# Kernel tuning notes

Measured on AMD Instinct MI355X. Metric: run time of the kernel, lower is better.

Reference implementation:

```python
import jax, jax.numpy as jnp
import numpy as np

KS = 3          # deform kernel size
N = KS * KS     # sampling points per output pixel
PAD = 1         # zero padding

def conv2d(x, w, stride, padding):
    return jax.lax.conv_general_dilated(
        x, w, (stride, stride), [(padding, padding), (padding, padding)],
        dimension_numbers=('NCHW', 'OIHW', 'NCHW'))

def _gather(x_flat, qx, qy, Wp):
    # x_flat: [b, c, Hp*Wp]; qx, qy: [b, h, w, N] int32 -> [b, c, h, w, N]
    b = qx.shape[0]; c = x_flat.shape[1]
    idx = (qx * Wp + qy).reshape(b, 1, -1)
    out = jnp.take_along_axis(x_flat, jnp.broadcast_to(idx, (b, c, idx.shape[-1])), axis=2)
    return out.reshape(b, c, qx.shape[1], qx.shape[2], qx.shape[3])

def deform_conv(x, w_off, b_off, w_conv):
    # learned per-pixel offsets: [b, 2N, h, w] (first N = x-offsets, last N = y-offsets)
    offset = conv2d(x, w_off, 1, PAD) + b_off[None, :, None, None]
    b, _, h, w = offset.shape
    x_pad = jnp.pad(x, ((0, 0), (0, 0), (PAD, PAD), (PAD, PAD)))
    Hp, Wp = x_pad.shape[2], x_pad.shape[3]
    # kernel-relative offsets p_n in {-1,0,1}^2
    pn_x, pn_y = jnp.meshgrid(jnp.arange(-(KS // 2), KS // 2 + 1),
                              jnp.arange(-(KS // 2), KS // 2 + 1), indexing='ij')
    p_n = jnp.concatenate([pn_x.reshape(-1), pn_y.reshape(-1)]).reshape(1, 2 * N, 1, 1)
    # base grid p_0 (1..h, 1..w in padded coordinates)
    p0_x, p0_y = jnp.meshgrid(jnp.arange(1, h + 1), jnp.arange(1, w + 1), indexing='ij')
    p_0 = jnp.concatenate([jnp.tile(p0_x[None], (N, 1, 1)),
                           jnp.tile(p0_y[None], (N, 1, 1))])[None]  # [1, 2N, h, w]
    p = (p_0 + p_n).astype(offset.dtype) + offset                   # [b, 2N, h, w]
    p = jnp.transpose(p, (0, 2, 3, 1))                              # [b, h, w, 2N]
    px, py = p[..., :N], p[..., N:]
    q = jnp.floor(jax.lax.stop_gradient(p))
    qlt_x = jnp.clip(q[..., :N], 0, Hp - 1); qlt_y = jnp.clip(q[..., N:], 0, Wp - 1)
    qrb_x = jnp.clip(q[..., :N] + 1, 0, Hp - 1); qrb_y = jnp.clip(q[..., N:] + 1, 0, Wp - 1)
    px = jnp.clip(px, 0, Hp - 1); py = jnp.clip(py, 0, Wp - 1)
    # bilinear weights (classic DCN formulation)
    g_lt = (1 + (qlt_x - px)) * (1 + (qlt_y - py))
    g_rb = (1 - (qrb_x - px)) * (1 - (qrb_y - py))
    g_lb = (1 + (qlt_x - px)) * (1 - (qrb_y - py))
    g_rt = (1 - (qrb_x - px)) * (1 + (qlt_y - py))
    x_flat = x_pad.reshape(b, x_pad.shape[1], -1)
    qi = lambda a: a.astype(jnp.int32)
    x_lt = _gather(x_flat, qi(qlt_x), qi(qlt_y), Wp)
    x_rb = _gather(x_flat, qi(qrb_x), qi(qrb_y), Wp)
    x_lb = _gather(x_flat, qi(qlt_x), qi(qrb_y), Wp)
    x_rt = _gather(x_flat, qi(qrb_x), qi(qlt_y), Wp)
    xo = (g_lt[:, None] * x_lt + g_rb[:, None] * x_rb
          + g_lb[:, None] * x_lb + g_rt[:, None] * x_rt)  # [b, c, h, w, N]
    c = xo.shape[1]
    # unfold N -> (ks, ks) blocks: [b, c, h*ks, w*ks]
    xo = xo.reshape(b, c, h, w, KS, KS).transpose(0, 1, 2, 4, 3, 5).reshape(b, c, h * KS, w * KS)
    return conv2d(xo, w_conv, KS, 0)  # stride=ks aggregation, no bias

def reference(x, w_off, b_off, w_conv, w_fc, b_fc):
    y = jax.nn.relu(deform_conv(x, w_off, b_off, w_conv))          # [b, 8, 28, 28]
    y = jax.lax.reduce_window(y, -jnp.inf, jax.lax.max,
                              (1, 1, 2, 2), (1, 1, 2, 2), 'VALID')  # [b, 8, 14, 14]
    y = y.reshape(y.shape[0], -1)
    return y @ w_fc.T + b_fc

def setup_inputs() -> dict:
    key = jax.random.key(0)
    k1, k2, k3, k4 = jax.random.split(key, 4)
    B = 4096
    return {
        'x': jax.random.normal(k1, (B, 1, 28, 28), dtype=jnp.float32),
        'w_off': jax.random.normal(k2, (18, 1, 3, 3), dtype=jnp.float32) * 0.1,
        'b_off': jnp.zeros((18,), dtype=jnp.float32),
        'w_conv': jax.random.normal(k3, (8, 1, 3, 3), dtype=jnp.float32) * 0.3,
        'w_fc': jax.random.normal(k4, (10, 8 * 14 * 14), dtype=jnp.float32) * 0.02,
        'b_fc': jnp.zeros((10,), dtype=jnp.float32),
    }
```

## Files before the change

### kernel.cpp

```cpp
#include <hip/hip_runtime.h>


#define HH 28
#define WW 28
#define WP 30
#define NPOS 784
#define NPOOL 1568
#define CELLS 196

__global__ __launch_bounds__(256) void deform_net_kernel(
    const float* __restrict__ x,
    const float* __restrict__ w_off,
    const float* __restrict__ b_off,
    const float* __restrict__ w_conv,
    const float* __restrict__ w_fc,
    const float* __restrict__ b_fc,
    float* __restrict__ out)
{
    __shared__ float xs[900];
    __shared__ float wo_s[162];
    __shared__ float bo_s[18];
    __shared__ float wc_s[72];
    __shared__ float red[4][10];

    const int b   = blockIdx.x;
    const int tid = threadIdx.x;

    if (tid < 162) wo_s[tid] = w_off[tid];
    if (tid < 18)  bo_s[tid] = b_off[tid];
    if (tid < 72)  wc_s[tid] = w_conv[tid];

    const float* xb = x + (size_t)b * NPOS;
    for (int i = tid; i < 900; i += 256) {
        int r = i / WP, c = i % WP;
        float v = 0.f;
        if (r >= 1 && r <= HH && c >= 1 && c <= WW)
            v = xb[(r - 1) * WW + (c - 1)];
        xs[i] = v;
    }
    __syncthreads();

    float fc[10];
    #pragma unroll
    for (int c = 0; c < 10; c++) fc[c] = 0.f;

    if (tid < CELLS) {
        const int ph = tid / 14, pw = tid % 14;
        const int h0 = 2 * ph, w0 = 2 * pw;

        float nb[16];
        #pragma unroll
        for (int i = 0; i < 4; i++)
            #pragma unroll
            for (int j = 0; j < 4; j++)
                nb[i * 4 + j] = xs[(h0 + i) * WP + (w0 + j)];

        float acc[4][8];
        #pragma unroll
        for (int p = 0; p < 4; p++)
            #pragma unroll
            for (int o = 0; o < 8; o++) acc[p][o] = 0.f;

        #pragma unroll
        for (int k = 0; k < 9; k++) {
            const int kx = k / 3, ky = k % 3;
            #pragma unroll
            for (int p = 0; p < 4; p++) {
                const int dh = p >> 1, dw = p & 1;

                float offx = bo_s[k], offy = bo_s[k + 9];
                #pragma unroll
                for (int t = 0; t < 9; t++) {
                    float nv = nb[(dh + t / 3) * 4 + (dw + t % 3)];
                    offx = fmaf(wo_s[k * 9 + t],       nv, offx);
                    offy = fmaf(wo_s[(k + 9) * 9 + t], nv, offy);
                }

                float p_x = (float)(h0 + dh + kx) + offx;
                float p_y = (float)(w0 + dw + ky) + offy;

                float q0x = floorf(p_x), q0y = floorf(p_y);
                float qltx = fminf(fmaxf(q0x,       0.f), 29.f);
                float qlty = fminf(fmaxf(q0y,       0.f), 29.f);
                float qrbx = fminf(fmaxf(q0x + 1.f, 0.f), 29.f);
                float qrby = fminf(fmaxf(q0y + 1.f, 0.f), 29.f);
                float px   = fminf(fmaxf(p_x,       0.f), 29.f);
                float py   = fminf(fmaxf(p_y,       0.f), 29.f);

                float gltx = 1.f + (qltx - px);
                float glty = 1.f + (qlty - py);
                float grbx = 1.f - (qrbx - px);
                float grby = 1.f - (qrby - py);

                int ilx = (int)qltx, ily = (int)qlty;
                int irx = (int)qrbx, iry = (int)qrby;

                float xlt = xs[ilx * WP + ily];
                float xrb = xs[irx * WP + iry];
                float xlb = xs[ilx * WP + iry];
                float xrt = xs[irx * WP + ily];

                float s = gltx * (glty * xlt + grby * xlb)
                        + grbx * (glty * xrt + grby * xrb);

                #pragma unroll
                for (int o = 0; o < 8; o++)
                    acc[p][o] = fmaf(wc_s[o * 9 + k], s, acc[p][o]);
            }
        }

        #pragma unroll
        for (int o = 0; o < 8; o++) {
            float m = fmaxf(fmaxf(acc[0][o], acc[1][o]),
                            fmaxf(acc[2][o], acc[3][o]));
            m = fmaxf(m, 0.f);
            const float* wrow = w_fc + o * CELLS + tid;
            #pragma unroll
            for (int c = 0; c < 10; c++)
                fc[c] = fmaf(m, wrow[c * NPOOL], fc[c]);
        }
    }

    #pragma unroll
    for (int c = 0; c < 10; c++) {
        #pragma unroll
        for (int sh = 32; sh > 0; sh >>= 1)
            fc[c] += __shfl_down(fc[c], sh, 64);
    }
    const int wave = tid >> 6, lane = tid & 63;
    if (lane == 0) {
        #pragma unroll
        for (int c = 0; c < 10; c++) red[wave][c] = fc[c];
    }
    __syncthreads();
    if (tid < 10)
        out[b * 10 + tid] = red[0][tid] + red[1][tid] + red[2][tid]
                          + red[3][tid] + b_fc[tid];
}

extern "C" void kernel_launch(void* const* d_in, const int* in_sizes, int n_in,
                              void* d_out, int out_size, void* d_ws, size_t ws_size,
                              hipStream_t stream) {
    const float* x      = (const float*)d_in[0];
    const float* w_off  = (const float*)d_in[1];
    const float* b_off  = (const float*)d_in[2];
    const float* w_conv = (const float*)d_in[3];
    const float* w_fc   = (const float*)d_in[4];
    const float* b_fc   = (const float*)d_in[5];
    float* out = (float*)d_out;

    const int B = in_sizes[0] / NPOS;
    deform_net_kernel<<<B, 256, 0, stream>>>(x, w_off, b_off, w_conv, w_fc, b_fc, out);
}
```

Before: 126.8 us.

## Pack pooled cells contiguously across images so every thread in a block works

Threads now map linearly onto global pooled-cell indices, so a 256-thread block covers cells from up to three images instead of leaving 60 of 256 threads idle per image. Each block stages up to three padded images in shared memory. The per-image FC sums are combined with wavefront shuffles and global atomicAdd into output zeroed by a memset. In exchange it adds atomics, a memset launch, more shared-memory staging per block, and a floating-point summation order that is no longer deterministic.

Result: slower. 144.2 us (+13.7%).

```diff
diff --git a/kernel.cpp b/kernel.cpp
--- a/kernel.cpp
+++ b/kernel.cpp
@@ -15,37 +15,49 @@
     const float* __restrict__ w_conv,
     const float* __restrict__ w_fc,
     const float* __restrict__ b_fc,
-    float* __restrict__ out)
+    float* __restrict__ out,
+    int B)
 {
-    __shared__ float xs[900];
+    __shared__ float xs[3 * 900];
     __shared__ float wo_s[162];
     __shared__ float bo_s[18];
     __shared__ float wc_s[72];
-    __shared__ float red[4][10];
 
-    const int b   = blockIdx.x;
-    const int tid = threadIdx.x;
+    const int tid      = threadIdx.x;
+    const int cell0    = blockIdx.x << 8;
+    const int img_base = cell0 / CELLS;
+    const int base_lc  = cell0 - img_base * CELLS;
 
     if (tid < 162) wo_s[tid] = w_off[tid];
     if (tid < 18)  bo_s[tid] = b_off[tid];
     if (tid < 72)  wc_s[tid] = w_conv[tid];
 
-    const float* xb = x + (size_t)b * NPOS;
-    for (int i = tid; i < 900; i += 256) {
-        int r = i / WP, c = i % WP;
+    for (int i = tid; i < 2700; i += 256) {
+        int s = i / 900;
+        int j = i - s * 900;
+        int img = img_base + s;
         float v = 0.f;
-        if (r >= 1 && r <= HH && c >= 1 && c <= WW)
-            v = xb[(r - 1) * WW + (c - 1)];
+        if (img < B) {
+            int r = j / WP, c = j - r * WP;
+            if (r >= 1 && r <= HH && c >= 1 && c <= WW)
+                v = x[(size_t)img * NPOS + (r - 1) * WW + (c - 1)];
+        }
         xs[i] = v;
     }
     __syncthreads();
+
+    const int lc   = base_lc + tid;
+    const int slot = (lc >= 2 * CELLS) ? 2 : (lc >= CELLS ? 1 : 0);
+    const int cell = lc - slot * CELLS;
+    const int xb0  = slot * 900;
+    const bool act = (cell0 + tid) < B * CELLS;
 
     float fc[10];
     #pragma unroll
     for (int c = 0; c < 10; c++) fc[c] = 0.f;
 
-    if (tid < CELLS) {
-        const int ph = tid / 14, pw = tid % 14;
+    if (act) {
+        const int ph = cell / 14, pw = cell % 14;
         const int h0 = 2 * ph, w0 = 2 * pw;
 
         float nb[16];
@@ -53,7 +65,7 @@
         for (int i = 0; i < 4; i++)
             #pragma unroll
             for (int j = 0; j < 4; j++)
-                nb[i * 4 + j] = xs[(h0 + i) * WP + (w0 + j)];
+                nb[i * 4 + j] = xs[xb0 + (h0 + i) * WP + (w0 + j)];
 
         float acc[4][8];
         #pragma unroll
@@ -95,10 +107,10 @@
                 int ilx = (int)qltx, ily = (int)qlty;
                 int irx = (int)qrbx, iry = (int)qrby;
 
-                float xlt = xs[ilx * WP + ily];
-                float xrb = xs[irx * WP + iry];
-                float xlb = xs[ilx * WP + iry];
-                float xrt = xs[irx * WP + ily];
+                float xlt = xs[xb0 + ilx * WP + ily];
+                float xrb = xs[xb0 + irx * WP + iry];
+                float xlb = xs[xb0 + ilx * WP + iry];
+                float xrt = xs[xb0 + irx * WP + ily];
 
                 float s = gltx * (glty * xlt + grby * xlb)
                         + grbx * (glty * xrt + grby * xrb);
@@ -114,28 +126,50 @@
             float m = fmaxf(fmaxf(acc[0][o], acc[1][o]),
                             fmaxf(acc[2][o], acc[3][o]));
             m = fmaxf(m, 0.f);
-            const float* wrow = w_fc + o * CELLS + tid;
+            const float* wrow = w_fc + o * CELLS + cell;
             #pragma unroll
             for (int c = 0; c < 10; c++)
                 fc[c] = fmaf(m, wrow[c * NPOOL], fc[c]);
         }
+        if (cell == 0) {
+            #pragma unroll
+            for (int c = 0; c < 10; c++) fc[c] += b_fc[c];
+        }
     }
 
-    #pragma unroll
-    for (int c = 0; c < 10; c++) {
+    const int lane = tid & 63;
+    const int wfl  = base_lc + (tid & ~63);
+    const int s0   = (wfl >= 2 * CELLS) ? 2 : (wfl >= CELLS ? 1 : 0);
+    const int wll  = wfl + 63;
+    const int s1   = (wll >= 2 * CELLS) ? 2 : (wll >= CELLS ? 1 : 0);
+    const int img0 = img_base + s0;
+    const int img1 = img_base + s1;
+
+    if (s0 == s1) {
         #pragma unroll
-        for (int sh = 32; sh > 0; sh >>= 1)
-            fc[c] += __shfl_down(fc[c], sh, 64);
+        for (int c = 0; c < 10; c++) {
+            float v = fc[c];
+            #pragma unroll
+            for (int sh = 32; sh > 0; sh >>= 1) v += __shfl_down(v, sh, 64);
+            if (lane == 0 && img0 < B) atomicAdd(&out[img0 * 10 + c], v);
+        }
+    } else {
+        const bool in0 = (slot == s0);
+        #pragma unroll
+        for (int c = 0; c < 10; c++) {
+            float v0 = in0 ? fc[c] : 0.f;
+            float v1 = fc[c] - v0;
+            #pragma unroll
+            for (int sh = 32; sh > 0; sh >>= 1) {
+                v0 += __shfl_down(v0, sh, 64);
+                v1 += __shfl_down(v1, sh, 64);
+            }
+            if (lane == 0) {
+                if (img0 < B) atomicAdd(&out[img0 * 10 + c], v0);
+                if (img1 < B) atomicAdd(&out[img1 * 10 + c], v1);
+            }
+        }
     }
-    const int wave = tid >> 6, lane = tid & 63;
-    if (lane == 0) {
-        #pragma unroll
-        for (int c = 0; c < 10; c++) red[wave][c] = fc[c];
-    }
-    __syncthreads();
-    if (tid < 10)
-        out[b * 10 + tid] = red[0][tid] + red[1][tid] + red[2][tid]
-                          + red[3][tid] + b_fc[tid];
 }
 
 extern "C" void kernel_launch(void* const* d_in, const int* in_sizes, int n_in,
@@ -150,5 +184,9 @@
     float* out = (float*)d_out;
 
     const int B = in_sizes[0] / NPOS;
-    deform_net_kernel<<<B, 256, 0, stream>>>(x, w_off, b_off, w_conv, w_fc, b_fc, out);
+    const int grid = (B * CELLS + 255) / 256;
+
+    hipMemsetAsync(d_out, 0, (size_t)out_size * sizeof(float), stream);
+    deform_net_kernel<<<grid, 256, 0, stream>>>(x, w_off, b_off, w_conv,
+                                                w_fc, b_fc, out, B);
 }
```
